# Optimization experiments

Measured on AMD Instinct MI355X. Metric: run time of the kernel, lower is better.

## Reference

```python
import jax, jax.numpy as jnp
import numpy as np

N = 100000      # nodes
E = 800000      # directed edges (self-loops added in reference, PyG default)
F_IN = 16
H1, C1 = 3, 32  # conv1: heads=3, out=32 (concat -> 96)
H2, C2 = 1, 32  # conv2: heads=1, out=32
NC = 16         # n_channel
SLOPE = 0.2     # PyG GATConv default negative_slope


def setup_inputs() -> dict:
    key = jax.random.key(0)
    ks = jax.random.split(key, 12)
    s = 0.1
    return {
        "x": jax.random.normal(ks[0], (N, F_IN), jnp.float32),
        "edge_index": jax.random.randint(ks[1], (2, E), 0, N, dtype=jnp.int32),
        "W1": jax.random.normal(ks[2], (F_IN, H1 * C1), jnp.float32) * s,
        "a_src1": jax.random.normal(ks[3], (H1, C1), jnp.float32) * s,
        "a_dst1": jax.random.normal(ks[4], (H1, C1), jnp.float32) * s,
        "b1": jnp.zeros((H1 * C1,), jnp.float32),
        "W2": jax.random.normal(ks[5], (H1 * C1, H2 * C2), jnp.float32) * s,
        "a_src2": jax.random.normal(ks[6], (H2, C2), jnp.float32) * s,
        "a_dst2": jax.random.normal(ks[7], (H2, C2), jnp.float32) * s,
        "b2": jnp.zeros((H2 * C2,), jnp.float32),
        "Wf": jax.random.normal(ks[8], (C2, NC), jnp.float32) * s,
        "bf": jnp.zeros((NC,), jnp.float32),
    }


def _gat_layer(x, src, dst, W, a_s, a_d, b, heads, outc):
    # x: [N, Fin]; src/dst: [Etot]
    h = (x @ W).reshape(N, heads, outc)                        # [N, H, C]
    alpha_s = (h * a_s).sum(-1)                                # [N, H]
    alpha_d = (h * a_d).sum(-1)                                # [N, H]
    e = jax.nn.leaky_relu(alpha_s[src] + alpha_d[dst], SLOPE)  # [Etot, H]
    # scatter-softmax over edges grouped by destination node
    m = jax.ops.segment_max(e, dst, num_segments=N)            # [N, H]
    p = jnp.exp(e - m[dst])
    z = jax.ops.segment_sum(p, dst, num_segments=N)
    alpha = p / (z[dst] + 1e-16)                               # [Etot, H]
    out = jax.ops.segment_sum(h[src] * alpha[:, :, None], dst, num_segments=N)
    return out.reshape(N, heads * outc) + b


def reference(x, edge_index, W1, a_src1, a_dst1, b1, W2, a_src2, a_dst2, b2, Wf, bf):
    loops = jnp.arange(N, dtype=edge_index.dtype)  # PyG add_self_loops=True
    src = jnp.concatenate([edge_index[0], loops])
    dst = jnp.concatenate([edge_index[1], loops])
    h = jax.nn.selu(_gat_layer(x, src, dst, W1, a_src1, a_dst1, b1, H1, C1))
    h = jax.nn.selu(_gat_layer(h, src, dst, W2, a_src2, a_dst2, b2, H2, C2))
    return h @ Wf + bf
```

## Files before the change

### kernel.cpp

```cpp
#include <hip/hip_runtime.h>
#include <hip/hip_bf16.h>

#define N_NODES 100000
#define N_EDGES 800000
#define F_IN    16
#define H1      3
#define C1      32
#define F1      (H1*C1)
#define F2      32
#define NC      16
#define SLOPE       0.2f
#define SELU_SCALE  1.0507009873554805f
#define SELU_ALPHA  1.6732632423543772f

#define DEG_PAD 32

#define NSLICE        8
#define BLK_PER_SLICE 256
#define SCAT_BLKS     (NSLICE * BLK_PER_SLICE)
#define EDGES_PER_BLK (N_EDGES / BLK_PER_SLICE)
#define SLICE_NODES   (N_NODES / NSLICE)
#define XB_NB   ((N_NODES + 255) / 256)
#define BIN_CAP 512

typedef unsigned short ushort_t;

__device__ __forceinline__ ushort_t f2bf(float f) {
    unsigned u = __float_as_uint(f);
    return (ushort_t)((u + 0x7FFFu + ((u >> 16) & 1u)) >> 16);
}
__device__ __forceinline__ unsigned pack2bf(float a, float b) {
    return (unsigned)f2bf(a) | ((unsigned)f2bf(b) << 16);
}
__device__ __forceinline__ float bf_lo(unsigned u) { return __uint_as_float(u << 16); }
__device__ __forceinline__ float bf_hi(unsigned u) { return __uint_as_float(u & 0xFFFF0000u); }

__device__ __forceinline__ void unpack8(const uint4 v, float* f) {
    f[0] = bf_lo(v.x); f[1] = bf_hi(v.x);
    f[2] = bf_lo(v.y); f[3] = bf_hi(v.y);
    f[4] = bf_lo(v.z); f[5] = bf_hi(v.z);
    f[6] = bf_lo(v.w); f[7] = bf_hi(v.w);
}
__device__ __forceinline__ float selu_f(float u) {
    return u > 0.f ? SELU_SCALE * u : SELU_SCALE * SELU_ALPHA * (__expf(u) - 1.f);
}

__global__ __launch_bounds__(256) void build_k(
    const int* __restrict__ ei, const float* __restrict__ x,
    const float* __restrict__ W1, const float* __restrict__ aS1,
    const float* __restrict__ aD1,
    int* __restrict__ deg, int* __restrict__ colp,
    uint4* __restrict__ xb, float4* __restrict__ as4, float4* __restrict__ ad4)
{
    __shared__ uint2 sbuf[BIN_CAP];
    __shared__ int scnt;
    __shared__ float swv[F_IN * 6];
    const int b = blockIdx.x, t = threadIdx.x;
    if (b < SCAT_BLKS) {
        if (t == 0) scnt = 0;
        __syncthreads();
        const int slice = b & 7;
        const int lo = slice * SLICE_NODES, hi = lo + SLICE_NODES;
        const int e0 = (b >> 3) * EDGES_PER_BLK;
        const int lane = t & 63;
        for (int e = e0 + t; e < e0 + EDGES_PER_BLK; e += 256) {
            const int d = ei[N_EDGES + e];
            const bool pred = (d >= lo) && (d < hi);
            const unsigned long long mask = __ballot(pred);
            if (mask) {
                const int leader = (int)(__ffsll((unsigned long long)mask) - 1);
                int base = 0;
                if (lane == leader) base = atomicAdd(&scnt, (int)__popcll(mask));
                base = __shfl(base, leader);
                if (pred) {
                    const int off = (int)__popcll(mask & ((1ull << lane) - 1ull));
                    const int pos = min(base + off, BIN_CAP - 1);
                    sbuf[pos] = make_uint2((unsigned)ei[e], (unsigned)(d - lo));
                }
            }
        }
        __syncthreads();
        const int n = min(scnt, BIN_CAP);
        int* cslice = colp + (size_t)slice * DEG_PAD * SLICE_NODES;
        for (int i = t; i < n; i += 256) {
            const uint2 e = sbuf[i];
            const int dl = (int)e.y;
            const int pos = atomicAdd(&deg[lo + dl], 1);
            if (pos < DEG_PAD) cslice[pos * SLICE_NODES + dl] = (int)e.x;
        }
    } else {
        if (t < 96) {
            const int k = t / 6, j = t % 6;
            const int h = (j < 3) ? j : j - 3;
            const float* a = (j < 3) ? aS1 : aD1;
            float acc = 0.f;
#pragma unroll
            for (int c = 0; c < 32; ++c) acc += W1[k * F1 + h * 32 + c] * a[h * 32 + c];
            swv[k * 6 + j] = acc;
        }
        __syncthreads();
        const int node = (b - SCAT_BLKS) * 256 + t;
        if (node < N_NODES) {
            float xr[16];
            const float4* xp = reinterpret_cast<const float4*>(&x[(size_t)node * F_IN]);
            const float4 v0 = xp[0], v1 = xp[1], v2 = xp[2], v3 = xp[3];
            xr[0] = v0.x; xr[1] = v0.y; xr[2]  = v0.z; xr[3]  = v0.w;
            xr[4] = v1.x; xr[5] = v1.y; xr[6]  = v1.z; xr[7]  = v1.w;
            xr[8] = v2.x; xr[9] = v2.y; xr[10] = v2.z; xr[11] = v2.w;
            xr[12] = v3.x; xr[13] = v3.y; xr[14] = v3.z; xr[15] = v3.w;
            uint4 o0, o1;
            o0.x = pack2bf(xr[0], xr[1]);   o0.y = pack2bf(xr[2], xr[3]);
            o0.z = pack2bf(xr[4], xr[5]);   o0.w = pack2bf(xr[6], xr[7]);
            o1.x = pack2bf(xr[8], xr[9]);   o1.y = pack2bf(xr[10], xr[11]);
            o1.z = pack2bf(xr[12], xr[13]); o1.w = pack2bf(xr[14], xr[15]);
            xb[(size_t)node * 2]     = o0;
            xb[(size_t)node * 2 + 1] = o1;
            float sacc[3] = {0.f, 0.f, 0.f}, dacc[3] = {0.f, 0.f, 0.f};
#pragma unroll
            for (int k = 0; k < 16; ++k) {
                const float xk = xr[k];
#pragma unroll
                for (int j = 0; j < 3; ++j) {
                    sacc[j] += xk * swv[k * 6 + j];
                    dacc[j] += xk * swv[k * 6 + 3 + j];
                }
            }
            as4[node] = make_float4(sacc[0], sacc[1], sacc[2], 0.f);
            ad4[node] = make_float4(dacc[0], dacc[1], dacc[2], 0.f);
        }
    }
}

__global__ __launch_bounds__(256) void agg1_l12_k(
    const int* __restrict__ deg, const int* __restrict__ colp,
    const uint4* __restrict__ xb,
    const float4* __restrict__ as4, const float4* __restrict__ ad4,
    const float* __restrict__ W1, const float* __restrict__ b1,
    const float* __restrict__ W2,
    const float* __restrict__ aS2, const float* __restrict__ aD2,
    ushort_t* __restrict__ h2b, float* __restrict__ as2, float* __restrict__ ad2)
{
    __shared__ unsigned sxap[64 * 24];
    __shared__ unsigned sx2p[64][49];
    __shared__ float swv[F1 * 2];
    const int t = threadIdx.x;
    const int node0 = blockIdx.x * 64;

    if (t < 192) {
        const int k = t >> 1, j = t & 1;
        const float* a = j ? aD2 : aS2;
        float acc = 0.f;
#pragma unroll
        for (int c = 0; c < 32; ++c) acc += W2[k * F2 + c] * a[c];
        swv[k * 2 + j] = acc;
    }

    {
        const int nl = t >> 2;
        const int node = node0 + nl;
        const int u = t & 1;
        const int v = (t >> 1) & 1;
        if (node < N_NODES) {
            const int slice = node / SLICE_NODES;
            const int dl = node - slice * SLICE_NODES;
            const int* cbase = colp + (size_t)slice * DEG_PAD * SLICE_NODES + dl;
            const int dg = min(deg[node], DEG_PAD);
            const float4 adv = ad4[node];
            float acc[3][8];
#pragma unroll
            for (int h = 0; h < 3; ++h)
#pragma unroll
                for (int i = 0; i < 8; ++i) acc[h][i] = 0.f;
            float z0 = 0.f, z1 = 0.f, z2 = 0.f;
            if (v == 0) {
                const float4 a = as4[node];
                float e0 = a.x + adv.x; e0 = e0 > 0.f ? e0 : SLOPE * e0;
                float e1 = a.y + adv.y; e1 = e1 > 0.f ? e1 : SLOPE * e1;
                float e2 = a.z + adv.z; e2 = e2 > 0.f ? e2 : SLOPE * e2;
                const float p0 = __expf(e0), p1 = __expf(e1), p2 = __expf(e2);
                z0 = p0; z1 = p1; z2 = p2;
                float xf[8]; unpack8(xb[(size_t)node * 2 + u], xf);
#pragma unroll
                for (int i = 0; i < 8; ++i) {
                    acc[0][i] = p0 * xf[i]; acc[1][i] = p1 * xf[i]; acc[2][i] = p2 * xf[i];
                }
            }
            int j = v; uint4 hv; float4 av;
            if (j < dg) { const int s = cbase[j * SLICE_NODES]; av = as4[s]; hv = xb[(size_t)s * 2 + u]; }
            while (j < dg) {
                const uint4 cx = hv; const float4 ca = av;
                const int jn = j + 2;
                if (jn < dg) {
                    const int s = cbase[jn * SLICE_NODES];
                    av = as4[s]; hv = xb[(size_t)s * 2 + u];
                }
                float e0 = ca.x + adv.x; e0 = e0 > 0.f ? e0 : SLOPE * e0;
                float e1 = ca.y + adv.y; e1 = e1 > 0.f ? e1 : SLOPE * e1;
                float e2 = ca.z + adv.z; e2 = e2 > 0.f ? e2 : SLOPE * e2;
                const float p0 = __expf(e0), p1 = __expf(e1), p2 = __expf(e2);
                z0 += p0; z1 += p1; z2 += p2;
                float xf[8]; unpack8(cx, xf);
#pragma unroll
                for (int i = 0; i < 8; ++i) {
                    acc[0][i] += p0 * xf[i]; acc[1][i] += p1 * xf[i]; acc[2][i] += p2 * xf[i];
                }
                j = jn;
            }
            z0 += __shfl_xor(z0, 2); z1 += __shfl_xor(z1, 2); z2 += __shfl_xor(z2, 2);
#pragma unroll
            for (int h = 0; h < 3; ++h)
#pragma unroll
                for (int i = 0; i < 8; ++i) acc[h][i] += __shfl_xor(acc[h][i], 2);
            if (v == 0) {
                const float zi[3] = {1.f / (z0 + 1e-16f), 1.f / (z1 + 1e-16f),
                                     1.f / (z2 + 1e-16f)};
#pragma unroll
                for (int h = 0; h < 3; ++h) {
                    uint4 o;
                    o.x = pack2bf(acc[h][0] * zi[h], acc[h][1] * zi[h]);
                    o.y = pack2bf(acc[h][2] * zi[h], acc[h][3] * zi[h]);
                    o.z = pack2bf(acc[h][4] * zi[h], acc[h][5] * zi[h]);
                    o.w = pack2bf(acc[h][6] * zi[h], acc[h][7] * zi[h]);
                    *reinterpret_cast<uint4*>(&sxap[nl * 24 + h * 8 + u * 4]) = o;
                }
            }
        } else if (v == 0) {
#pragma unroll
            for (int h = 0; h < 3; ++h)
                *reinterpret_cast<uint4*>(&sxap[nl * 24 + h * 8 + u * 4]) =
                    make_uint4(0, 0, 0, 0);
        }
    }
    __syncthreads();

    for (int tt = t; tt < 384; tt += 256) {
        const int ng = tt / 48;
        const int cp = tt - ng * 48;
        const int c0 = cp * 2, c1 = c0 + 1;
        const int hc = c0 >> 5;
        float w0[16], w1[16];
#pragma unroll
        for (int k = 0; k < 16; ++k) { w0[k] = W1[k * F1 + c0]; w1[k] = W1[k * F1 + c1]; }
        const float bc0 = b1[c0], bc1 = b1[c1];
#pragma unroll
        for (int nn = 0; nn < 8; ++nn) {
            const int n = ng * 8 + nn;
            const uint4* xp = reinterpret_cast<const uint4*>(&sxap[n * 24 + hc * 8]);
            float xa[16];
            unpack8(xp[0], xa);
            unpack8(xp[1], xa + 8);
            float acc0 = bc0, acc1 = bc1;
#pragma unroll
            for (int k = 0; k < 16; ++k) { acc0 += xa[k] * w0[k]; acc1 += xa[k] * w1[k]; }
            sx2p[n][cp] = pack2bf(selu_f(acc0), selu_f(acc1));
        }
    }
    __syncthreads();

    {
        const int cq = t & 7;
        const int np = t >> 3;
        const int n0 = np * 2, n1 = n0 + 1;
        float acc0[4] = {0.f, 0.f, 0.f, 0.f}, acc1[4] = {0.f, 0.f, 0.f, 0.f};
        float s0 = 0.f, s1 = 0.f;
        const int wj = cq & 1;
#pragma unroll 4
        for (int jk = 0; jk < 48; ++jk) {
            const unsigned u0 = sx2p[n0][jk];
            const unsigned u1 = sx2p[n1][jk];
            const float xe0 = bf_lo(u0), xo0 = bf_hi(u0);
            const float xe1 = bf_lo(u1), xo1 = bf_hi(u1);
            const float4 we = *reinterpret_cast<const float4*>(&W2[(2 * jk) * F2 + cq * 4]);
            const float4 wo = *reinterpret_cast<const float4*>(&W2[(2 * jk + 1) * F2 + cq * 4]);
            acc0[0] += xe0 * we.x + xo0 * wo.x; acc0[1] += xe0 * we.y + xo0 * wo.y;
            acc0[2] += xe0 * we.z + xo0 * wo.z; acc0[3] += xe0 * we.w + xo0 * wo.w;
            acc1[0] += xe1 * we.x + xo1 * wo.x; acc1[1] += xe1 * we.y + xo1 * wo.y;
            acc1[2] += xe1 * we.z + xo1 * wo.z; acc1[3] += xe1 * we.w + xo1 * wo.w;
            if (cq < 2) {
                s0 += xe0 * swv[(2 * jk) * 2 + wj] + xo0 * swv[(2 * jk + 1) * 2 + wj];
                s1 += xe1 * swv[(2 * jk) * 2 + wj] + xo1 * swv[(2 * jk + 1) * 2 + wj];
            }
        }
        if (node0 + n0 < N_NODES) {
            uint2 o; o.x = pack2bf(acc0[0], acc0[1]); o.y = pack2bf(acc0[2], acc0[3]);
            *reinterpret_cast<uint2*>(&h2b[(size_t)(node0 + n0) * F2 + cq * 4]) = o;
        }
        if (node0 + n1 < N_NODES) {
            uint2 o; o.x = pack2bf(acc1[0], acc1[1]); o.y = pack2bf(acc1[2], acc1[3]);
            *reinterpret_cast<uint2*>(&h2b[(size_t)(node0 + n1) * F2 + cq * 4]) = o;
        }
        if (cq < 2) {
            if (cq == 0) {
                if (node0 + n0 < N_NODES) as2[node0 + n0] = s0;
                if (node0 + n1 < N_NODES) as2[node0 + n1] = s1;
            } else {
                if (node0 + n0 < N_NODES) ad2[node0 + n0] = s0;
                if (node0 + n1 < N_NODES) ad2[node0 + n1] = s1;
            }
        }
    }
}

__global__ __launch_bounds__(256) void agg2_final_k(
    const int* __restrict__ deg, const int* __restrict__ colp,
    const ushort_t* __restrict__ hb,
    const float* __restrict__ as, const float* __restrict__ ad,
    const float* __restrict__ b2, const float* __restrict__ Wf,
    const float* __restrict__ bf, float* __restrict__ out)
{
    __shared__ float sW[F2 * NC];
    __shared__ float sx[64][33];
    const int t = threadIdx.x;
    for (int i = t; i < F2 * NC; i += 256) sW[i] = Wf[i];
    const int sub = t >> 2;
    const int u = t & 1;
    const int v = (t >> 1) & 1;
    const int node = blockIdx.x * 64 + sub;
    const bool valid = node < N_NODES;

    if (valid) {
        const int slice = node / SLICE_NODES;
        const int dl = node - slice * SLICE_NODES;
        const int* cbase = colp + (size_t)slice * DEG_PAD * SLICE_NODES + dl;
        const int dg = min(deg[node], DEG_PAD);
        const float adv = ad[node];
        float acc[16];
#pragma unroll
        for (int i = 0; i < 16; ++i) acc[i] = 0.f;
        float z = 0.f;
        if (v == 0) {
            float e = as[node] + adv; e = e > 0.f ? e : SLOPE * e;
            const float pv = __expf(e);
            z = pv;
            const uint4* hp = reinterpret_cast<const uint4*>(&hb[(size_t)node * F2 + u * 16]);
            float xf[8];
            unpack8(hp[0], xf);
#pragma unroll
            for (int i = 0; i < 8; ++i) acc[i] = pv * xf[i];
            unpack8(hp[1], xf);
#pragma unroll
            for (int i = 0; i < 8; ++i) acc[8 + i] = pv * xf[i];
        }
        int j = v; uint4 hva, hvb; float asv;
        if (j < dg) {
            const int s = cbase[j * SLICE_NODES];
            asv = as[s];
            const uint4* hp = reinterpret_cast<const uint4*>(&hb[(size_t)s * F2 + u * 16]);
            hva = hp[0]; hvb = hp[1];
        }
        while (j < dg) {
            const uint4 ca = hva, cb = hvb; const float cas = asv;
            const int jn = j + 2;
            if (jn < dg) {
                const int s = cbase[jn * SLICE_NODES];
                asv = as[s];
                const uint4* hp = reinterpret_cast<const uint4*>(&hb[(size_t)s * F2 + u * 16]);
                hva = hp[0]; hvb = hp[1];
            }
            float e = cas + adv; e = e > 0.f ? e : SLOPE * e;
            const float pv = __expf(e);
            z += pv;
            float xf[8];
            unpack8(ca, xf);
#pragma unroll
            for (int i = 0; i < 8; ++i) acc[i] += pv * xf[i];
            unpack8(cb, xf);
#pragma unroll
            for (int i = 0; i < 8; ++i) acc[8 + i] += pv * xf[i];
            j = jn;
        }
        z += __shfl_xor(z, 2);
#pragma unroll
        for (int i = 0; i < 16; ++i) acc[i] += __shfl_xor(acc[i], 2);
        if (v == 0) {
            const float zi = 1.f / (z + 1e-16f);
#pragma unroll
            for (int i = 0; i < 16; ++i)
                sx[sub][u * 16 + i] = selu_f(acc[i] * zi + b2[u * 16 + i]);
        }
    }
    __syncthreads();
    if (valid) {
        const int c0 = (t & 3) * 4;
        float r[4];
#pragma unroll
        for (int i = 0; i < 4; ++i) r[i] = bf[c0 + i];
#pragma unroll
        for (int k = 0; k < F2; ++k) {
            const float xk = sx[sub][k];
#pragma unroll
            for (int i = 0; i < 4; ++i) r[i] += xk * sW[k * NC + c0 + i];
        }
        *reinterpret_cast<float4*>(&out[(size_t)node * NC + c0]) =
            make_float4(r[0], r[1], r[2], r[3]);
    }
}

extern "C" void kernel_launch(void* const* d_in, const int* in_sizes, int n_in,
                              void* d_out, int out_size, void* d_ws, size_t ws_size,
                              hipStream_t stream)
{
    const float* x    = (const float*)d_in[0];
    const int*   ei   = (const int*)d_in[1];
    const float* W1   = (const float*)d_in[2];
    const float* aS1  = (const float*)d_in[3];
    const float* aD1  = (const float*)d_in[4];
    const float* b1   = (const float*)d_in[5];
    const float* W2   = (const float*)d_in[6];
    const float* aS2  = (const float*)d_in[7];
    const float* aD2  = (const float*)d_in[8];
    const float* b2   = (const float*)d_in[9];
    const float* Wf   = (const float*)d_in[10];
    const float* bf   = (const float*)d_in[11];
    float* out = (float*)d_out;

    uint4*    xb   = (uint4*)d_ws;
    float4*   as4  = (float4*)(xb + (size_t)N_NODES * 2);
    float4*   ad4  = as4 + N_NODES;
    ushort_t* h2b  = (ushort_t*)(ad4 + N_NODES);
    float*    as2  = (float*)(h2b + (size_t)N_NODES * F2);
    float*    ad2  = as2 + N_NODES;
    int*      colp = (int*)(ad2 + N_NODES);
    int*      deg  = colp + (size_t)N_NODES * DEG_PAD;

    hipMemsetAsync(deg, 0, sizeof(int) * N_NODES, stream);
    build_k<<<SCAT_BLKS + XB_NB, 256, 0, stream>>>(
        ei, x, W1, aS1, aD1, deg, colp, xb, as4, ad4);
    agg1_l12_k<<<(N_NODES + 63) / 64, 256, 0, stream>>>(
        deg, colp, xb, as4, ad4, W1, b1, W2, aS2, aD2, h2b, as2, ad2);
    agg2_final_k<<<(N_NODES + 63) / 64, 256, 0, stream>>>(
        deg, colp, h2b, as2, ad2, b2, Wf, bf, out);
}
```

Before: 139.9 us.

## Interleave per-node features and attention scores into 64-byte records; deepen gather prefetch

```diff
diff --git a/kernel.cpp b/kernel.cpp
--- a/kernel.cpp
+++ b/kernel.cpp
@@ -50,7 +50,7 @@
     const float* __restrict__ W1, const float* __restrict__ aS1,
     const float* __restrict__ aD1,
     int* __restrict__ deg, int* __restrict__ colp,
-    uint4* __restrict__ xb, float4* __restrict__ as4, float4* __restrict__ ad4)
+    uint4* __restrict__ rec4)
 {
     __shared__ uint2 sbuf[BIN_CAP];
     __shared__ int scnt;
@@ -113,8 +113,6 @@
             o0.z = pack2bf(xr[4], xr[5]);   o0.w = pack2bf(xr[6], xr[7]);
             o1.x = pack2bf(xr[8], xr[9]);   o1.y = pack2bf(xr[10], xr[11]);
             o1.z = pack2bf(xr[12], xr[13]); o1.w = pack2bf(xr[14], xr[15]);
-            xb[(size_t)node * 2]     = o0;
-            xb[(size_t)node * 2 + 1] = o1;
             float sacc[3] = {0.f, 0.f, 0.f}, dacc[3] = {0.f, 0.f, 0.f};
 #pragma unroll
             for (int k = 0; k < 16; ++k) {
@@ -125,16 +123,20 @@
                     dacc[j] += xk * swv[k * 6 + 3 + j];
                 }
             }
-            as4[node] = make_float4(sacc[0], sacc[1], sacc[2], 0.f);
-            ad4[node] = make_float4(dacc[0], dacc[1], dacc[2], 0.f);
+            uint4* dst = &rec4[(size_t)node * 4];
+            dst[0] = o0;
+            dst[1] = o1;
+            float4 sa = make_float4(sacc[0], sacc[1], sacc[2], 0.f);
+            float4 da = make_float4(dacc[0], dacc[1], dacc[2], 0.f);
+            dst[2] = *reinterpret_cast<uint4*>(&sa);
+            dst[3] = *reinterpret_cast<uint4*>(&da);
         }
     }
 }
 
 __global__ __launch_bounds__(256) void agg1_l12_k(
     const int* __restrict__ deg, const int* __restrict__ colp,
-    const uint4* __restrict__ xb,
-    const float4* __restrict__ as4, const float4* __restrict__ ad4,
+    const uint4* __restrict__ rec4,
     const float* __restrict__ W1, const float* __restrict__ b1,
     const float* __restrict__ W2,
     const float* __restrict__ aS2, const float* __restrict__ aD2,
@@ -145,6 +147,7 @@
     __shared__ float swv[F1 * 2];
     const int t = threadIdx.x;
     const int node0 = blockIdx.x * 64;
+    const float4* recf = reinterpret_cast<const float4*>(rec4);
 
     if (t < 192) {
         const int k = t >> 1, j = t & 1;
@@ -165,7 +168,7 @@
             const int dl = node - slice * SLICE_NODES;
             const int* cbase = colp + (size_t)slice * DEG_PAD * SLICE_NODES + dl;
             const int dg = min(deg[node], DEG_PAD);
-            const float4 adv = ad4[node];
+            const float4 adv = recf[(size_t)node * 4 + 3];
             float acc[3][8];
 #pragma unroll
             for (int h = 0; h < 3; ++h)
@@ -173,26 +176,35 @@
                 for (int i = 0; i < 8; ++i) acc[h][i] = 0.f;
             float z0 = 0.f, z1 = 0.f, z2 = 0.f;
             if (v == 0) {
-                const float4 a = as4[node];
+                const float4 a = recf[(size_t)node * 4 + 2];
                 float e0 = a.x + adv.x; e0 = e0 > 0.f ? e0 : SLOPE * e0;
                 float e1 = a.y + adv.y; e1 = e1 > 0.f ? e1 : SLOPE * e1;
                 float e2 = a.z + adv.z; e2 = e2 > 0.f ? e2 : SLOPE * e2;
                 const float p0 = __expf(e0), p1 = __expf(e1), p2 = __expf(e2);
                 z0 = p0; z1 = p1; z2 = p2;
-                float xf[8]; unpack8(xb[(size_t)node * 2 + u], xf);
+                float xf[8]; unpack8(rec4[(size_t)node * 4 + u], xf);
 #pragma unroll
                 for (int i = 0; i < 8; ++i) {
                     acc[0][i] = p0 * xf[i]; acc[1][i] = p1 * xf[i]; acc[2][i] = p2 * xf[i];
                 }
             }
-            int j = v; uint4 hv; float4 av;
-            if (j < dg) { const int s = cbase[j * SLICE_NODES]; av = as4[s]; hv = xb[(size_t)s * 2 + u]; }
+            int j = v;
+            uint4 hv0, hv1; float4 av0, av1;
+            if (j < dg) {
+                const int s = cbase[j * SLICE_NODES];
+                av0 = recf[(size_t)s * 4 + 2]; hv0 = rec4[(size_t)s * 4 + u];
+            }
+            if (j + 2 < dg) {
+                const int s = cbase[(j + 2) * SLICE_NODES];
+                av1 = recf[(size_t)s * 4 + 2]; hv1 = rec4[(size_t)s * 4 + u];
+            }
             while (j < dg) {
-                const uint4 cx = hv; const float4 ca = av;
-                const int jn = j + 2;
-                if (jn < dg) {
-                    const int s = cbase[jn * SLICE_NODES];
-                    av = as4[s]; hv = xb[(size_t)s * 2 + u];
+                const uint4 cx = hv0; const float4 ca = av0;
+                hv0 = hv1; av0 = av1;
+                const int jf = j + 4;
+                if (jf < dg) {
+                    const int s = cbase[jf * SLICE_NODES];
+                    av1 = recf[(size_t)s * 4 + 2]; hv1 = rec4[(size_t)s * 4 + u];
                 }
                 float e0 = ca.x + adv.x; e0 = e0 > 0.f ? e0 : SLOPE * e0;
                 float e1 = ca.y + adv.y; e1 = e1 > 0.f ? e1 : SLOPE * e1;
@@ -204,7 +216,7 @@
                 for (int i = 0; i < 8; ++i) {
                     acc[0][i] += p0 * xf[i]; acc[1][i] += p1 * xf[i]; acc[2][i] += p2 * xf[i];
                 }
-                j = jn;
+                j += 2;
             }
             z0 += __shfl_xor(z0, 2); z1 += __shfl_xor(z1, 2); z2 += __shfl_xor(z2, 2);
 #pragma unroll
@@ -341,21 +353,29 @@
 #pragma unroll
             for (int i = 0; i < 8; ++i) acc[8 + i] = pv * xf[i];
         }
-        int j = v; uint4 hva, hvb; float asv;
+        int j = v;
+        uint4 a0v, b0v, a1v, b1v; float s0v, s1v;
         if (j < dg) {
             const int s = cbase[j * SLICE_NODES];
-            asv = as[s];
+            s0v = as[s];
             const uint4* hp = reinterpret_cast<const uint4*>(&hb[(size_t)s * F2 + u * 16]);
-            hva = hp[0]; hvb = hp[1];
+            a0v = hp[0]; b0v = hp[1];
+        }
+        if (j + 2 < dg) {
+            const int s = cbase[(j + 2) * SLICE_NODES];
+            s1v = as[s];
+            const uint4* hp = reinterpret_cast<const uint4*>(&hb[(size_t)s * F2 + u * 16]);
+            a1v = hp[0]; b1v = hp[1];
         }
         while (j < dg) {
-            const uint4 ca = hva, cb = hvb; const float cas = asv;
-            const int jn = j + 2;
-            if (jn < dg) {
-                const int s = cbase[jn * SLICE_NODES];
-                asv = as[s];
+            const uint4 ca = a0v, cb = b0v; const float cas = s0v;
+            a0v = a1v; b0v = b1v; s0v = s1v;
+            const int jf = j + 4;
+            if (jf < dg) {
+                const int s = cbase[jf * SLICE_NODES];
+                s1v = as[s];
                 const uint4* hp = reinterpret_cast<const uint4*>(&hb[(size_t)s * F2 + u * 16]);
-                hva = hp[0]; hvb = hp[1];
+                a1v = hp[0]; b1v = hp[1];
             }
             float e = cas + adv; e = e > 0.f ? e : SLOPE * e;
             const float pv = __expf(e);
@@ -367,7 +387,7 @@
             unpack8(cb, xf);
 #pragma unroll
             for (int i = 0; i < 8; ++i) acc[8 + i] += pv * xf[i];
-            j = jn;
+            j += 2;
         }
         z += __shfl_xor(z, 2);
 #pragma unroll
@@ -414,10 +434,8 @@
     const float* bf   = (const float*)d_in[11];
     float* out = (float*)d_out;
 
-    uint4*    xb   = (uint4*)d_ws;
-    float4*   as4  = (float4*)(xb + (size_t)N_NODES * 2);
-    float4*   ad4  = as4 + N_NODES;
-    ushort_t* h2b  = (ushort_t*)(ad4 + N_NODES);
+    uint4*    rec4 = (uint4*)d_ws;
+    ushort_t* h2b  = (ushort_t*)(rec4 + (size_t)N_NODES * 4);
     float*    as2  = (float*)(h2b + (size_t)N_NODES * F2);
     float*    ad2  = as2 + N_NODES;
     int*      colp = (int*)(ad2 + N_NODES);
@@ -425,9 +443,9 @@
 
     hipMemsetAsync(deg, 0, sizeof(int) * N_NODES, stream);
     build_k<<<SCAT_BLKS + XB_NB, 256, 0, stream>>>(
-        ei, x, W1, aS1, aD1, deg, colp, xb, as4, ad4);
+        ei, x, W1, aS1, aD1, deg, colp, rec4);
     agg1_l12_k<<<(N_NODES + 63) / 64, 256, 0, stream>>>(
-        deg, colp, xb, as4, ad4, W1, b1, W2, aS2, aD2, h2b, as2, ad2);
+        deg, colp, rec4, W1, b1, W2, aS2, aD2, h2b, as2, ad2);
     agg2_final_k<<<(N_NODES + 63) / 64, 256, 0, stream>>>(
         deg, colp, h2b, as2, ad2, b2, Wf, bf, out);
 }
```

Result: faster. 135.3 us (-3.3%).
